# Optimization experiments

Hardware: AMD Instinct MI355X
Metric: run time of the kernel (lower is better)

The kernel has to match this reference:

```python
import jax
import jax.numpy as jnp
from jax import lax
import numpy as np

EPS = 1e-5
CLASS_COUNT = 1000

# conv specs: (out_c, in_c, k, pool_stride)
_SPECS = [(8, 1, 11, 1), (32, 8, 7, 2), (64, 32, 5, 2), (64, 64, 5, 2), (128, 64, 5, 2), (128, 128, 3, 2)]


def _maxpool3(x, stride):
    return lax.reduce_window(x, -jnp.inf, lax.max, (1, 1, 3, 3), (1, 1, stride, stride), 'VALID')


def _block(x, w, gamma, beta, pool_stride):
    # tanh soft-binarized weights (mode=1, w=1)
    wq = jnp.tanh(w)
    y = lax.conv_general_dilated(x, wq, (1, 1), 'VALID', dimension_numbers=('NCHW', 'OIHW', 'NCHW'))
    y = _maxpool3(y, pool_stride)
    # BatchNorm2d in training mode: batch statistics over (N,H,W), biased var
    mu = jnp.mean(y, axis=(0, 2, 3), keepdims=True)
    var = jnp.var(y, axis=(0, 2, 3), keepdims=True)
    y = (y - mu) * lax.rsqrt(var + EPS)
    y = y * gamma.reshape(1, -1, 1, 1) + beta.reshape(1, -1, 1, 1)
    # tanh soft-binarized activation (mode=1, w=1)
    return jnp.tanh(y)


def setup_inputs() -> dict:
    key = jax.random.key(0)
    keys = jax.random.split(key, 8)
    inp = {'x': jax.random.normal(keys[0], (128, 1, 227, 227), dtype=jnp.float32)}
    for i, (oc, ic, k, _) in enumerate(_SPECS):
        fan_in = ic * k * k
        inp[f'w{i+1}'] = jax.random.normal(keys[i + 1], (oc, ic, k, k), dtype=jnp.float32) / np.sqrt(fan_in)
        inp[f'g{i+1}'] = jnp.ones((oc,), dtype=jnp.float32)
        inp[f'b{i+1}'] = jnp.zeros((oc,), dtype=jnp.float32)
    inp['wl'] = jax.random.normal(keys[7], (CLASS_COUNT, 512), dtype=jnp.float32) / np.sqrt(512.0)
    return inp


def reference(x, w1, w2, w3, w4, w5, w6, g1, g2, g3, g4, g5, g6,
              b1, b2, b3, b4, b5, b6, wl):
    ws = (w1, w2, w3, w4, w5, w6)
    gs = (g1, g2, g3, g4, g5, g6)
    bs = (b1, b2, b3, b4, b5, b6)
    for i, (_, _, _, ps) in enumerate(_SPECS):
        x = _block(x, ws[i], gs[i], bs[i], ps)
    # flatten -> BinaryLinear (tanh-binarized weight, no bias)
    x = x.reshape(x.shape[0], -1)  # [B, 512]
    return x @ jnp.tanh(wl).T  # [B, classCount]
```

## Files before the change

kernel.cpp:

```cpp
#include <hip/hip_runtime.h>
#include <hip/hip_bf16.h>
#include <hip/hip_fp16.h>

using bf16 = __hip_bfloat16;
using f16  = _Float16;
using f16x8 = __attribute__((ext_vector_type(8))) _Float16;
using f32x4  = __attribute__((ext_vector_type(4))) float;
typedef unsigned long long u64;

__device__ __forceinline__ float b2f(bf16 v){ return __bfloat162float(v); }
__device__ __forceinline__ bf16 f2b(float v){ return __float2bfloat16(v); }
__device__ __forceinline__ float ldf(const float* p){ return *p; }
__device__ __forceinline__ float ldf(const bf16* p){ return b2f(*p); }
__device__ __forceinline__ float ldf(const __half* p){ return __half2float(*p); }
__device__ __forceinline__ void stf(float* p, float v){ *p = v; }
__device__ __forceinline__ void stf(bf16* p, float v){ *p = f2b(v); }
__device__ __forceinline__ void stf(__half* p, float v){ *p = __float2half(v); }

__device__ __forceinline__ float ftanh(float x){
    float t = __builtin_amdgcn_exp2f(x * 2.8853900817779268f);
    return 1.0f - 2.0f * __builtin_amdgcn_rcpf(t + 1.0f);
}

__device__ __forceinline__ float ld_any(const void* p, int i, int isBf16)
{
    return isBf16 ? b2f(((const bf16*)p)[i]) : ((const float*)p)[i];
}

__device__ __forceinline__ int det_bf(const void* g)
{
    return (*(const unsigned*)g == 0x3F803F80u) ? 1 : 0;
}

__device__ __forceinline__ void bn_pr(const float* __restrict__ sums,
                                      const void* __restrict__ g,
                                      const void* __restrict__ b,
                                      int bf, int C, float inv, int c,
                                      float& sc, float& sh)
{
    float mean = sums[c] * inv;
    float var  = sums[C + c] * inv - mean * mean;
    float rstd = rsqrtf(fmaxf(var, 0.f) + 1e-5f);
    sc = ld_any(g, c, bf) * rstd;
    sh = ld_any(b, c, bf) - mean * sc;
}

__global__ void xconv(const void* __restrict__ xin, float* __restrict__ xf,
                      const void* __restrict__ g1, int* __restrict__ flag, int n)
{
    int bf = det_bf(g1);
    int i = blockIdx.x * blockDim.x + threadIdx.x;
    if (i == 0) *flag = bf;
    if (i < n) xf[i] = ld_any(xin, i, bf);
}

__global__ __launch_bounds__(256)
void prep_all(const void* __restrict__ w1, const void* __restrict__ w6,
              const void* __restrict__ wlw, const void* __restrict__ w2,
              const void* __restrict__ w3, const void* __restrict__ w4,
              const void* __restrict__ w5, const void* __restrict__ g1,
              float* __restrict__ wq0, float* __restrict__ wq5,
              float* __restrict__ wlqT, __half* __restrict__ wpk,
              __half* __restrict__ wpk3, __half* __restrict__ wpk4,
              __half* __restrict__ wpk5)
{
    const int bf = det_bf(g1);
    const int b = blockIdx.x, t = threadIdx.x;
    if (b < 4) {
        int i = b * 256 + t;
        if (i < 968) wq0[i] = tanhf(ld_any(w1, i, bf));
    } else if (b < 580) {
        int i = (b - 4) * 256 + t;
        if (i < 147456) wq5[i] = tanhf(ld_any(w6, i, bf));
    } else if (b < 2580) {
        int i = (b - 580) * 256 + t;
        if (i < 512000) {
            int cls = i >> 9, k = i & 511;
            wlqT[k * 1000 + cls] = tanhf(ld_any(wlw, i, bf));
        }
    } else if (b < 2636) {
        int i = (b - 2580) * 256 + t;
        if (i < 14336) {
            int ic  = i & 7;
            int q   = (i >> 3) & 3;
            int col = (i >> 5) & 15;
            int g   = (i >> 9) & 1;
            int khg = (i >> 10) & 1;
            int kw  = i >> 11;
            int kh  = khg * 4 + q;
            int oc  = g * 16 + col;
            __half v = __float2half(0.f);
            if (kh < 7)
                v = __float2half(tanhf(ld_any(w2, (oc * 8 + ic) * 49 + kh * 7 + kw, bf)));
            wpk[i] = v;
        }
    } else if (b < 2836) {
        int i = (b - 2636) * 256 + t;
        if (i < 51200) {
            int tap = i >> 11;
            int g   = (i >> 9) & 3;
            int col = (i >> 5) & 15;
            int icp = i & 31;
            int oc  = g * 16 + col;
            wpk3[i] = __float2half(tanhf(ld_any(w3, (oc * 32 + icp) * 25 + tap, bf)));
        }
    } else if (b < 3236) {
        int i = (b - 2836) * 256 + t;
        if (i < 102400) {
            int step = i >> 11;
            int g    = (i >> 9) & 3;
            int col  = (i >> 5) & 15;
            int icp  = i & 31;
            int icg  = step / 25, tap = step - icg * 25;
            int oc   = g * 16 + col;
            int ic   = icg * 32 + icp;
            wpk4[i] = __float2half(tanhf(ld_any(w4, (oc * 64 + ic) * 25 + tap, bf)));
        }
    } else {
        int i = (b - 3236) * 256 + t;
        if (i < 204800) {
            int step = i >> 12;
            int ocg  = (i >> 11) & 1;
            int g    = (i >> 9) & 3;
            int col  = (i >> 5) & 15;
            int icp  = i & 31;
            int icg  = step / 25, tap = step - icg * 25;
            int oc   = ocg * 64 + g * 16 + col;
            int ic   = icg * 32 + icp;
            wpk5[i] = __float2half(tanhf(ld_any(w5, (oc * 64 + ic) * 25 + tap, bf)));
        }
    }
}

__global__ __launch_bounds__(256)
void b2conv(const __half* __restrict__ A1, const __half* __restrict__ wpk,
            __half* __restrict__ raw, float* __restrict__ sums2,
            const float* __restrict__ sums1, const void* __restrict__ g1,
            const void* __restrict__ b1)
{
    __shared__ __align__(16) char smem[32000];
    __shared__ float s_part[512];
    f16*   xs = (f16*)smem;
    float* pb = (float*)smem;

    const int tid = threadIdx.x;
    const int n   = blockIdx.z;
    const int ty  = blockIdx.x / 15, tx = blockIdx.x - ty * 15;
    const int cy0 = ty * 30, cx0 = tx * 14;

    const int bf1 = det_bf(g1);
    float ssc[8], ssh[8];
    #pragma unroll
    for (int j = 0; j < 8; j++)
        bn_pr(sums1, g1, b1, bf1, 8, 1.f / 5916800.f, j, ssc[j], ssh[j]);

    for (int i = tid; i < 858; i += 256) {
        int r = i / 22, c = i - r * 22;
        int gr = cy0 + r, gc = cx0 + c;
        f16x8 v = (f16x8){0, 0, 0, 0, 0, 0, 0, 0};
        if (gr < 215 && gc < 215)
            v = *(const f16x8*)((const f16*)A1 + ((size_t)(n * 215 + gr) * 215 + gc) * 8);
        f16x8 o;
        #pragma unroll
        for (int j = 0; j < 8; j++)
            o[j] = (f16)ftanh(fmaf((float)v[j], ssc[j], ssh[j]));
        *(f16x8*)(xs + i * 8) = o;
    }
    __syncthreads();

    const int lane = tid & 63, wid = tid >> 6;
    const int col = lane & 15, q = lane >> 4;
    const int arow = q * 22;

    f32x4 acc[8][2];
    #pragma unroll
    for (int f = 0; f < 8; f++)
        #pragma unroll
        for (int g = 0; g < 2; g++)
            acc[f][g] = (f32x4){0.f, 0.f, 0.f, 0.f};

    const f16* wb = (const f16*)wpk + col * 32 + q * 8;
    f16x8 wc0 = *(const f16x8*)(wb);
    f16x8 wc1 = *(const f16x8*)(wb + 512);

    #pragma unroll
    for (int s = 0; s < 14; s++) {
        f16x8 wn0 = wc0, wn1 = wc1;
        if (s < 13) {
            const f16* wn = wb + (s + 1) * 1024;
            wn0 = *(const f16x8*)(wn);
            wn1 = *(const f16x8*)(wn + 512);
        }
        int kw = s >> 1, khg = s & 1;
        int aoffs = arow + khg * 88 + kw;
        #pragma unroll
        for (int f = 0; f < 8; f++) {
            int gi = (wid * 8 + f) * 22 + col + aoffs;
            f16x8 a = *(const f16x8*)(xs + gi * 8);
            acc[f][0] = __builtin_amdgcn_mfma_f32_16x16x32_f16(a, wc0, acc[f][0], 0, 0, 0);
            acc[f][1] = __builtin_amdgcn_mfma_f32_16x16x32_f16(a, wc1, acc[f][1], 0, 0, 0);
        }
        wc0 = wn0; wc1 = wn1;
    }
    __syncthreads();

    for (int h = 0; h < 2; h++) {
        #pragma unroll
        for (int f = 0; f < 8; f++) {
            int cr = wid * 8 + f;
            if (cr < 31)
                *(f32x4*)(pb + col * 500 + cr * 16 + q * 4) = acc[f][h];
        }
        __syncthreads();
        const int ocl = tid >> 4, slot = tid & 15;
        float sm = 0.f, sq = 0.f;
        for (int j = slot; j < 105; j += 16) {
            int py = j / 7, px = j - (j / 7) * 7;
            int gph = ty * 15 + py, gpw = tx * 7 + px;
            if (gph < 104 && gpw < 104) {
                const float* cp = pb + ocl * 500 + (2 * py) * 16 + 2 * px;
                float m = cp[0];
                #pragma unroll
                for (int dy = 0; dy < 3; dy++)
                    #pragma unroll
                    for (int dx = 0; dx < 3; dx++)
                        m = fmaxf(m, cp[dy * 16 + dx]);
                int oc = h * 16 + ocl;
                size_t oidx = ((size_t)(n * 104 + gph) * 104 + gpw) * 32 + oc;
                raw[oidx] = __float2half(m);
                sm += m; sq += m * m;
            }
        }
        s_part[tid] = sm; s_part[256 + tid] = sq;
        __syncthreads();
        if (tid < 16) {
            float a = 0.f, b = 0.f;
            #pragma unroll
            for (int t = 0; t < 16; t++) {
                a += s_part[tid * 16 + t];
                b += s_part[256 + tid * 16 + t];
            }
            atomicAdd(&sums2[h * 16 + tid],      a);
            atomicAdd(&sums2[32 + h * 16 + tid], b);
        }
        __syncthreads();
    }
}

__global__ __launch_bounds__(256)
void b3conv(const __half* __restrict__ A2, const __half* __restrict__ wpk3,
            float* __restrict__ A3, float* __restrict__ sums3,
            const float* __restrict__ sums2, const void* __restrict__ g2,
            const void* __restrict__ b2)
{
    __shared__ __align__(16) char smem[32000];
    __shared__ float s_part[512];
    f16*   xs = (f16*)smem;
    float* pb = (float*)smem;

    const int tid = threadIdx.x;
    const int n   = blockIdx.z;
    const int ty  = blockIdx.x / 7, tx = blockIdx.x - ty * 7;
    const int y0  = ty * 14, x0 = tx * 14;

    if (tid < 32) {
        float sc, sh;
        bn_pr(sums2, g2, b2, det_bf(g2), 32, 1.f / 1384448.f, tid, sc, sh);
        s_part[tid] = sc; s_part[32 + tid] = sh;
    }
    __syncthreads();

    for (int i = tid; i < 1600; i += 256) {
        int pos = i >> 2, g8 = i & 3;
        int gy = y0 + pos / 20, gx = x0 + pos % 20;
        f16x8 v = *(const f16x8*)((const f16*)A2 +
                  ((size_t)(n * 104 + gy) * 104 + gx) * 32 + g8 * 8);
        int c0 = g8 * 8;
        f16x8 o;
        #pragma unroll
        for (int j = 0; j < 8; j++)
            o[j] = (f16)ftanh(fmaf((float)v[j], s_part[c0 + j], s_part[32 + c0 + j]));
        *(f16x8*)(xs + pos * 40 + g8 * 8) = o;
    }

    const int lane = tid & 63, wid = tid >> 6;
    const int col = lane & 15, q = lane >> 4;

    f32x4 acc[4][4];
    #pragma unroll
    for (int f = 0; f < 4; f++)
        #pragma unroll
        for (int g = 0; g < 4; g++)
            acc[f][g] = (f32x4){0.f, 0.f, 0.f, 0.f};

    const f16* wb = (const f16*)wpk3 + col * 32 + q * 8;
    f16x8 w[4];
    #pragma unroll
    for (int g = 0; g < 4; g++)
        w[g] = *(const f16x8*)(wb + g * 512);

    __syncthreads();

    #pragma unroll 1
    for (int tap = 0; tap < 25; tap++) {
        const f16* wnb = wb + (tap < 24 ? tap + 1 : tap) * 2048;
        f16x8 wn[4];
        #pragma unroll
        for (int g = 0; g < 4; g++)
            wn[g] = *(const f16x8*)(wnb + g * 512);

        int kh = tap / 5, kw = tap - (tap / 5) * 5;
        f16x8 a[4];
        #pragma unroll
        for (int f = 0; f < 4; f++) {
            int pos = (wid * 4 + f + kh) * 20 + col + kw;
            a[f] = *(const f16x8*)(xs + pos * 40 + q * 8);
        }
        #pragma unroll
        for (int g = 0; g < 4; g++)
            #pragma unroll
            for (int f = 0; f < 4; f++)
                acc[f][g] = __builtin_amdgcn_mfma_f32_16x16x32_f16(
                    a[f], w[g], acc[f][g], 0, 0, 0);
        #pragma unroll
        for (int g = 0; g < 4; g++)
            w[g] = wn[g];
    }

    for (int h = 0; h < 2; h++) {
        __syncthreads();
        #pragma unroll
        for (int f = 0; f < 4; f++) {
            int cr = wid * 4 + f;
            if (cr < 15) {
                #pragma unroll
                for (int gg = 0; gg < 2; gg++)
                    *(f32x4*)(pb + (gg * 16 + col) * 244 + cr * 16 + q * 4) = acc[f][h * 2 + gg];
            }
        }
        __syncthreads();
        const int ocl = tid >> 3, slot = tid & 7;
        float sm = 0.f, sq = 0.f;
        for (int j = slot; j < 49; j += 8) {
            int py = j / 7, px = j - (j / 7) * 7;
            const float* cp = pb + ocl * 244 + (2 * py) * 16 + 2 * px;
            float m = cp[0];
            #pragma unroll
            for (int dy = 0; dy < 3; dy++)
                #pragma unroll
                for (int dx = 0; dx < 3; dx++)
                    m = fmaxf(m, cp[dy * 16 + dx]);
            A3[((size_t)(n * 64 + h * 32 + ocl) * 49 + ty * 7 + py) * 49 + tx * 7 + px] = m;
            sm += m; sq += m * m;
        }
        s_part[tid] = sm; s_part[256 + tid] = sq;
        __syncthreads();
        if (tid < 32) {
            float a = 0.f, b = 0.f;
            #pragma unroll
            for (int t = 0; t < 8; t++) {
                a += s_part[tid * 8 + t];
                b += s_part[256 + tid * 8 + t];
            }
            atomicAdd(&sums3[h * 32 + tid],      a);
            atomicAdd(&sums3[64 + h * 32 + tid], b);
        }
    }
}

__global__ __launch_bounds__(256)
void bn_tanh_h_t(const float* __restrict__ x, __half* __restrict__ out,
                 const float* __restrict__ sums3, const void* __restrict__ g3,
                 const void* __restrict__ b3)
{
    __shared__ float tile[64][50];
    __shared__ float s_ss[128];
    const int tid = threadIdx.x;
    const int h = blockIdx.x % 49;
    const int n = blockIdx.x / 49;
    const int c = tid >> 2, j = tid & 3;
    if (tid < 64) {
        float sc, sh;
        bn_pr(sums3, g3, b3, det_bf(g3), 64, 1.f / 307328.f, tid, sc, sh);
        s_ss[tid] = sc; s_ss[64 + tid] = sh;
    }
    const float* xp = x + ((size_t)(n * 64 + c) * 49 + h) * 49;
    for (int w = j; w < 49; w += 4)
        tile[c][w] = xp[w];
    __syncthreads();
    __half* op = out + ((size_t)(n * 49 + h) * 49) * 64;
    for (int pos = tid; pos < 49 * 64; pos += 256) {
        int w = pos >> 6, cc = pos & 63;
        op[pos] = __float2half(ftanh(fmaf(tile[cc][w], s_ss[cc], s_ss[64 + cc])));
    }
}

__global__ __launch_bounds__(256)
void bn4_apply(const float* __restrict__ x, __half* __restrict__ out,
               const float* __restrict__ sums4, const void* __restrict__ g4,
               const void* __restrict__ b4)
{
    __shared__ float s_ss[128];
    int tid = threadIdx.x;
    if (tid < 64) {
        float sc, sh;
        bn_pr(sums4, g4, b4, det_bf(g4), 64, 1.f / 61952.f, tid, sc, sh);
        s_ss[tid] = sc; s_ss[64 + tid] = sh;
    }
    __syncthreads();
    int idx = blockIdx.x * 256 + tid;
    if (idx >= 3964928) return;
    int w  = idx % 22;
    int t1 = idx / 22;
    int h  = t1 % 22;
    int t2 = t1 / 22;
    int c  = t2 & 63;
    int n  = t2 >> 6;
    float t = ftanh(fmaf(x[idx], s_ss[c], s_ss[64 + c]));
    out[((size_t)(n * 22 + h) * 22 + w) * 64 + c] = __float2half(t);
}

__global__ __launch_bounds__(256)
void b4conv(const __half* __restrict__ A3t, const __half* __restrict__ wpk4,
            float* __restrict__ A4, float* __restrict__ sums4)
{
    __shared__ __align__(16) char smem[31232];
    __shared__ float s_part[512];
    f16*   xs = (f16*)smem;
    float* pb = (float*)smem;

    const int tid = threadIdx.x;
    const int n   = blockIdx.z;
    const int ty  = blockIdx.x >> 2, tx = blockIdx.x & 3;
    const int y0  = ty * 14, x0 = tx * 14;
    const int lane = tid & 63, wid = tid >> 6;
    const int col = lane & 15, q = lane >> 4;

    f32x4 acc[4][4];
    #pragma unroll
    for (int f = 0; f < 4; f++)
        #pragma unroll
        for (int g = 0; g < 4; g++)
            acc[f][g] = (f32x4){0.f, 0.f, 0.f, 0.f};

    const f16* wb = (const f16*)wpk4 + col * 32 + q * 8;
    f16x8 w[4];
    #pragma unroll
    for (int g = 0; g < 4; g++)
        w[g] = *(const f16x8*)(wb + g * 512);

    #pragma unroll 1
    for (int icg = 0; icg < 2; icg++) {
        __syncthreads();
        for (int i = tid; i < 1520; i += 256) {
            int pos = i >> 2, g8 = i & 3;
            int gy = y0 + pos / 20, gx = x0 + pos % 20;
            f16x8 v = (f16x8){0, 0, 0, 0, 0, 0, 0, 0};
            if (gy < 49 && gx < 49)
                v = *(const f16x8*)((const f16*)A3t +
                    ((size_t)(n * 49 + gy) * 49 + gx) * 64 + icg * 32 + g8 * 8);
            *(f16x8*)(xs + pos * 40 + g8 * 8) = v;
        }
        __syncthreads();

        #pragma unroll 1
        for (int tap = 0; tap < 25; tap++) {
            int step = icg * 25 + tap;
            const f16* wnb = wb + (size_t)(step < 49 ? step + 1 : step) * 2048;
            f16x8 wn[4];
            #pragma unroll
            for (int g = 0; g < 4; g++)
                wn[g] = *(const f16x8*)(wnb + g * 512);

            int kh = tap / 5, kw = tap - (tap / 5) * 5;
            f16x8 a[4];
            #pragma unroll
            for (int f = 0; f < 4; f++) {
                int r = wid * 4 + f + kh; if (r > 18) r = 18;
                int pos = r * 20 + col + kw;
                a[f] = *(const f16x8*)(xs + pos * 40 + q * 8);
            }
            #pragma unroll
            for (int g = 0; g < 4; g++)
                #pragma unroll
                for (int f = 0; f < 4; f++)
                    acc[f][g] = __builtin_amdgcn_mfma_f32_16x16x32_f16(
                        a[f], w[g], acc[f][g], 0, 0, 0);
            #pragma unroll
            for (int g = 0; g < 4; g++)
                w[g] = wn[g];
        }
    }

    for (int h = 0; h < 2; h++) {
        __syncthreads();
        #pragma unroll
        for (int f = 0; f < 4; f++) {
            int cr = wid * 4 + f;
            if (cr < 15) {
                #pragma unroll
                for (int gg = 0; gg < 2; gg++)
                    *(f32x4*)(pb + (gg * 16 + col) * 244 + cr * 16 + q * 4) = acc[f][h * 2 + gg];
            }
        }
        __syncthreads();
        const int ocl = tid >> 3, slot = tid & 7;
        float sm = 0.f, sq = 0.f;
        for (int j = slot; j < 49; j += 8) {
            int py = j / 7, px = j - (j / 7) * 7;
            int gph = ty * 7 + py, gpw = tx * 7 + px;
            if (gph < 22 && gpw < 22) {
                const float* cp = pb + ocl * 244 + (2 * py) * 16 + 2 * px;
                float m = cp[0];
                #pragma unroll
                for (int dy = 0; dy < 3; dy++)
                    #pragma unroll
                    for (int dx = 0; dx < 3; dx++)
                        m = fmaxf(m, cp[dy * 16 + dx]);
                A4[((size_t)(n * 64 + h * 32 + ocl) * 22 + gph) * 22 + gpw] = m;
                sm += m; sq += m * m;
            }
        }
        s_part[tid] = sm; s_part[256 + tid] = sq;
        __syncthreads();
        if (tid < 32) {
            float a = 0.f, b = 0.f;
            #pragma unroll
            for (int t = 0; t < 8; t++) {
                a += s_part[tid * 8 + t];
                b += s_part[256 + tid * 8 + t];
            }
            atomicAdd(&sums4[h * 32 + tid],      a);
            atomicAdd(&sums4[64 + h * 32 + tid], b);
        }
    }
}

__global__ __launch_bounds__(256)
void b5conv(const __half* __restrict__ A4t, const __half* __restrict__ wpk5,
            float* __restrict__ A5, float* __restrict__ sums5)
{
    __shared__ __align__(16) char smem[49664];
    __shared__ float s_part[512];
    f16*   xs = (f16*)smem;
    float* pb = (float*)smem;

    const int tid = threadIdx.x;
    const int n   = blockIdx.z;
    const int ocg = blockIdx.x;
    const int lane = tid & 63, wid = tid >> 6;
    const int col = lane & 15, q = lane >> 4;

    int abase[6];
    #pragma unroll
    for (int f = 0; f < 6; f++) {
        int m = (wid * 6 + f) * 16 + col;
        if (m > 323) m = 323;
        int r = m / 18, cc = m - r * 18;
        abase[f] = r * 22 + cc;
    }

    f32x4 acc[6][4];
    #pragma unroll
    for (int f = 0; f < 6; f++)
        #pragma unroll
        for (int g = 0; g < 4; g++)
            acc[f][g] = (f32x4){0.f, 0.f, 0.f, 0.f};

    const f16* wb = (const f16*)wpk5 + ocg * 2048 + col * 32 + q * 8;
    f16x8 w[4];
    #pragma unroll
    for (int g = 0; g < 4; g++)
        w[g] = *(const f16x8*)(wb + g * 512);

    #pragma unroll 1
    for (int icg = 0; icg < 2; icg++) {
        __syncthreads();
        for (int i = tid; i < 1936; i += 256) {
            int pos = i >> 2, g8 = i & 3;
            *(f16x8*)(xs + pos * 40 + g8 * 8) =
                *(const f16x8*)((const f16*)A4t + ((size_t)(n * 484 + pos)) * 64
                                + icg * 32 + g8 * 8);
        }
        __syncthreads();

        #pragma unroll 1
        for (int tap = 0; tap < 25; tap++) {
            int step = icg * 25 + tap;
            const f16* wnb = wb + (size_t)(step < 49 ? step + 1 : step) * 4096;
            f16x8 wn[4];
            #pragma unroll
            for (int g = 0; g < 4; g++)
                wn[g] = *(const f16x8*)(wnb + g * 512);

            int kh = tap / 5, kw = tap - (tap / 5) * 5;
            int off = kh * 22 + kw;
            f16x8 a[6];
            #pragma unroll
            for (int f = 0; f < 6; f++)
                a[f] = *(const f16x8*)(xs + (abase[f] + off) * 40 + q * 8);
            #pragma unroll
            for (int g = 0; g < 4; g++)
                #pragma unroll
                for (int f = 0; f < 6; f++)
                    acc[f][g] = __builtin_amdgcn_mfma_f32_16x16x32_f16(
                        a[f], w[g], acc[f][g], 0, 0, 0);
            #pragma unroll
            for (int g = 0; g < 4; g++)
                w[g] = wn[g];
        }
    }

    for (int h = 0; h < 2; h++) {
        __syncthreads();
        #pragma unroll
        for (int f = 0; f < 6; f++)
            #pragma unroll
            for (int gg = 0; gg < 2; gg++)
                *(f32x4*)(pb + (gg * 16 + col) * 388 + (wid * 6 + f) * 16 + q * 4)
                    = acc[f][h * 2 + gg];
        __syncthreads();
        const int ocl = tid >> 3, slot = tid & 7;
        float sm = 0.f, sq = 0.f;
        for (int j = slot; j < 64; j += 8) {
            int py = j >> 3, px = j & 7;
            const float* cp = pb + ocl * 388 + (2 * py) * 18 + 2 * px;
            float m = cp[0];
            #pragma unroll
            for (int dy = 0; dy < 3; dy++)
                #pragma unroll
                for (int dx = 0; dx < 3; dx++)
                    m = fmaxf(m, cp[dy * 18 + dx]);
            int oc = ocg * 64 + h * 32 + ocl;
            A5[((size_t)(n * 128 + oc) * 8 + py) * 8 + px] = m;
            sm += m; sq += m * m;
        }
        s_part[tid] = sm; s_part[256 + tid] = sq;
        __syncthreads();
        if (tid < 32) {
            float a = 0.f, b = 0.f;
            #pragma unroll
            for (int t = 0; t < 8; t++) {
                a += s_part[tid * 8 + t];
                b += s_part[256 + tid * 8 + t];
            }
            int oc = ocg * 64 + h * 32 + tid;
            atomicAdd(&sums5[oc],       a);
            atomicAdd(&sums5[128 + oc], b);
        }
    }
}

template<int MODE, int IC, int OC, int K, int PS, int TPH, int TPW,
         int OCB, int OCT, int CIC, int NP, bool ONHWC, typename InT, typename OutT>
__global__ __launch_bounds__(256)
void ctile(const InT* __restrict__ in, const float* __restrict__ wq,
           OutT* __restrict__ out, float* __restrict__ sums,
           const float* __restrict__ ss,
           int Hin, int Win, int PH, int PW, int tilesX)
{
    constexpr int TPO  = OCB / OCT;
    constexpr int CH   = PS * (TPH - 1) + 3;
    constexpr int CW   = PS * (TPW - 1) + 3;
    constexpr int SPR  = (CW + NP - 1) / NP;
    constexpr int CWP  = SPR * NP;
    constexpr int NSTR = CH * SPR;
    static_assert(NSTR * TPO <= 256, "thread mapping overflow");
    constexpr int IH   = CH + K - 1;
    constexpr int IW   = CW + K - 1;
    constexpr int IWE_ = (CWP + K - 1 > IW) ? (CWP + K - 1) : IW;
    constexpr int IWE  = IWE_ | 1;
    constexpr int IN_SZ  = CIC * IH * IWE;
    constexpr int INP    = (IN_SZ + 3) & ~3;
    constexpr int W_SZ   = CIC * K * K * OCB;
    constexpr int CONV_SZ = OCB * CH * CWP;
    constexpr int LDS_SZ = (INP + W_SZ > CONV_SZ) ? (INP + W_SZ) : CONV_SZ;

    __shared__ __align__(16) float lds[LDS_SZ];
    __shared__ float s_part[512];

    const int tid = threadIdx.x;
    const int n   = blockIdx.z;
    const int oc0 = blockIdx.y * OCB;
    const int tY  = blockIdx.x / tilesX;
    const int tX  = blockIdx.x - tY * tilesX;
    const int ph0 = tY * TPH, pw0 = tX * TPW;
    const int ih0 = ph0 * PS, iw0 = pw0 * PS;

    const int  og  = tid % TPO;
    const int  s   = tid / TPO;
    const bool act = (s < NSTR);
    const int  r   = s / SPR;
    const int  c0  = (s - r * SPR) * NP;

    float acc[NP][OCT];
    #pragma unroll
    for (int p = 0; p < NP; p++)
        #pragma unroll
        for (int o = 0; o < OCT; o++) acc[p][o] = 0.f;

    for (int icb = 0; icb < IC; icb += CIC) {
        for (int idx = tid; idx < IN_SZ; idx += 256) {
            int ic  = idx / (IH * IWE);
            int rem = idx - ic * (IH * IWE);
            int rr  = rem / IWE, cc = rem - rr * IWE;
            int gr  = ih0 + rr, gc = iw0 + cc;
            float v = 0.f;
            if (gr < Hin && gc < Win)
                v = ldf(&in[((size_t)(n * IC + icb + ic) * Hin + gr) * Win + gc]);
            lds[idx] = v;
        }
        for (int idx = tid; idx < W_SZ; idx += 256) {
            int ocl = idx % OCB;
            int kk  = (idx / OCB) % (K * K);
            int c_  = idx / (OCB * K * K);
            lds[INP + idx] = wq[((size_t)(oc0 + ocl) * IC + icb + c_) * (K * K) + kk];
        }
        __syncthreads();

        if (act) {
            #pragma unroll 1
            for (int ic_ = 0; ic_ < CIC; ic_++) {
                const float* xb = lds + ic_ * (IH * IWE);
                const float* wb = lds + INP + ic_ * (K * K * OCB) + og * OCT;
                #pragma unroll 1
                for (int kh = 0; kh < K; kh++) {
                    const float* xr = xb + (r + kh) * IWE + c0;
                    float xwin[NP + K - 1];
                    #pragma unroll
                    for (int j = 0; j < NP + K - 1; j++) xwin[j] = xr[j];
                    #pragma unroll
                    for (int kw = 0; kw < K; kw++) {
                        const float* wp2 = wb + (kh * K + kw) * OCB;
                        float wv[OCT];
                        #pragma unroll
                        for (int o = 0; o < OCT; o += 4) {
                            float4 t = *(const float4*)(wp2 + o);
                            wv[o] = t.x; wv[o+1] = t.y; wv[o+2] = t.z; wv[o+3] = t.w;
                        }
                        #pragma unroll
                        for (int p = 0; p < NP; p++)
                            #pragma unroll
                            for (int o = 0; o < OCT; o++)
                                acc[p][o] = fmaf(wv[o], xwin[p + kw], acc[p][o]);
                    }
                }
            }
        }
        __syncthreads();
    }

    if (act) {
        #pragma unroll
        for (int p = 0; p < NP; p++)
            #pragma unroll
            for (int o = 0; o < OCT; o++)
                lds[(og * OCT + o) * (CH * CWP) + r * CWP + c0 + p] = acc[p][o];
    }
    __syncthreads();

    {
        constexpr int TPC = 256 / OCB;
        const int ocl = tid / TPC, slot = tid - ocl * TPC;
        float sm = 0.f, sq = 0.f;
        for (int j = slot; j < TPH * TPW; j += TPC) {
            int py = j / TPW, px = j - (j / TPW) * TPW;
            int gph = ph0 + py, gpw = pw0 + px;
            if (gph < PH && gpw < PW) {
                const float* cp = lds + ocl * (CH * CWP) + (py * PS) * CWP + px * PS;
                float m = cp[0];
                #pragma unroll
                for (int dy = 0; dy < 3; dy++)
                    #pragma unroll
                    for (int dx = 0; dx < 3; dx++)
                        m = fmaxf(m, cp[dy * CWP + dx]);
                size_t oidx = ONHWC
                    ? ((size_t)(n * PH + gph) * PW + gpw) * OC + oc0 + ocl
                    : ((size_t)(n * OC + oc0 + ocl) * PH + gph) * PW + gpw;
                if (MODE == 2) {
                    int c = oc0 + ocl;
                    stf(&out[oidx], ftanh(fmaf(m, ss[c], ss[OC + c])));
                } else {
                    if (MODE == 0) stf(&out[oidx], m);
                    sm += m; sq += m * m;
                }
            }
        }
        if (MODE != 2) {
            s_part[tid] = sm; s_part[256 + tid] = sq;
            __syncthreads();
            if (tid < OCB) {
                float a = 0.f, b = 0.f;
// ... 87 lines not shown
    __shared__ float ls[256], ls2[256];
    ls[threadIdx.x] = s; ls2[threadIdx.x] = s2;
    __syncthreads();
    for (int w = 128; w > 0; w >>= 1) {
        if (threadIdx.x < w) {
            ls[threadIdx.x]  += ls[threadIdx.x + w];
            ls2[threadIdx.x] += ls2[threadIdx.x + w];
        }
        __syncthreads();
    }
    if (threadIdx.x == 0) {
        atomicAdd(&sums[c],     ls[0]);
        atomicAdd(&sums[C + c], ls2[0]);
    }
}

__global__ __launch_bounds__(256)
void bn_tanh_p(float* __restrict__ x, const float* __restrict__ sums,
               const void* __restrict__ g, const void* __restrict__ b,
               int C, int PHW, float invCnt)
{
    int plane = blockIdx.y;
    int c = plane & (C - 1);
    float sc, sh;
    bn_pr(sums, g, b, det_bf(g), C, invCnt, c, sc, sh);
    float* xp = x + (long)plane * PHW;
    for (int i = blockIdx.x * 256 + threadIdx.x; i < PHW; i += 256 * gridDim.x)
        xp[i] = ftanh(fmaf(xp[i], sc, sh));
}

__global__ __launch_bounds__(256)
void linear_k(const float* __restrict__ act, const float* __restrict__ wlqT,
              void* __restrict__ out, const int* __restrict__ flag)
{
    __shared__ float s_a[512];
    int bf = *flag;
    int n = blockIdx.y;
    for (int i = threadIdx.x; i < 512; i += 256) s_a[i] = act[n * 512 + i];
    __syncthreads();
    int cls = blockIdx.x * 256 + threadIdx.x;
    if (cls < 1000) {
        float acc = 0.f;
        #pragma unroll 8
        for (int k = 0; k < 512; k++)
            acc = fmaf(s_a[k], wlqT[k * 1000 + cls], acc);
        if (bf) ((bf16*)out)[n * 1000 + cls] = f2b(acc);
        else    ((float*)out)[n * 1000 + cls] = acc;
    }
}

extern "C" void kernel_launch(void* const* d_in, const int* in_sizes, int n_in,
                              void* d_out, int out_size, void* d_ws, size_t ws_size,
                              hipStream_t stream)
{
    (void)in_sizes; (void)n_in; (void)out_size; (void)ws_size;
    const void* x = d_in[0];
    const void* W[6]; const void* G[6]; const void* B[6];
    for (int i = 0; i < 6; i++) {
        W[i] = d_in[1 + 3 * i];
        G[i] = d_in[2 + 3 * i];
        B[i] = d_in[3 + 3 * i];
    }
    const void* wl = d_in[19];

    char* p = (char*)d_ws;
    auto carve = [&](size_t bytes) -> void* {
        void* r = (void*)p;
        p += (bytes + 255) & ~((size_t)255);
        return r;
    };
    int*   flag = (int*)carve(256);
    const int wsz[6] = {968, 12544, 51200, 102400, 204800, 147456};
    float* wq[6];
    for (int i = 0; i < 6; i++) wq[i] = (float*)carve((size_t)wsz[i] * 4);
    float* wlqT = (float*)carve((size_t)512000 * 4);
    float* sums_all = (float*)carve(1536 * 4);
    float* S1 = sums_all;        float* S2 = sums_all + 256;
    float* S3 = sums_all + 512;  float* S4 = sums_all + 768;
    float* S5 = sums_all + 1024; float* S6 = sums_all + 1280;
    __half* wpk  = (__half*)carve((size_t)14336 * 2);
    __half* wpk3 = (__half*)carve((size_t)51200 * 2);
    __half* wpk4 = (__half*)carve((size_t)102400 * 2);
    __half* wpk5 = (__half*)carve((size_t)204800 * 2);
    float* xf   = (float*)carve((size_t)6595712 * 4);
    __half* A1  = (__half*)carve((size_t)47334400 * 2);
    __half* A2  = (__half*)carve((size_t)44302336 * 2);
    float*  A3  = (float*)A1;
    __half* A3t = (__half*)A2;
    float*  A4  = (float*)A1;
    float*  A5  = (float*)A2;
    __half* A4t = (__half*)((char*)A2 + (size_t)16 * 1024 * 1024);
    float*  A6  = (float*)A1;

    auto cdiv = [](int a, int b) { return (a + b - 1) / b; };

    hipMemsetAsync(sums_all, 0, 1536 * 4, stream);
    xconv<<<cdiv(6595712, 256), 256, 0, stream>>>(x, xf, G[0], flag, 6595712);
    prep_all<<<4036, 256, 0, stream>>>(W[0], W[5], wl, W[1], W[2], W[3], W[4], G[0],
                                       wq[0], wq[5], wlqT, wpk, wpk3, wpk4, wpk5);

    ctile<0, 1, 8, 11, 1, 34, 40, 8, 8, 1, 7, true, float, __half>
        <<<dim3(42, 1, 128), 256, 0, stream>>>(xf, wq[0], A1, S1, S1, 227, 227, 215, 215, 6);

    b2conv<<<dim3(105, 1, 128), 256, 0, stream>>>(A1, wpk, A2, S2, S1, G[0], B[0]);

    b3conv<<<dim3(49, 1, 128), 256, 0, stream>>>(A2, wpk3, A3, S3, S2, G[1], B[1]);
    bn_tanh_h_t<<<128 * 49, 256, 0, stream>>>(A3, A3t, S3, G[2], B[2]);

    b4conv<<<dim3(16, 1, 128), 256, 0, stream>>>(A3t, wpk4, A4, S4);
    bn4_apply<<<cdiv(3964928, 256), 256, 0, stream>>>(A4, A4t, S4, G[3], B[3]);

    b5conv<<<dim3(2, 1, 128), 256, 0, stream>>>(A4t, wpk5, A5, S5);
    bn_tanh_p<<<dim3(1, 16384), 256, 0, stream>>>(A5, S5, G[4], B[4], 128, 64, 1.f / 8192.f);

    {
        int total = 65536;
        convpool<3, 0, float, float><<<cdiv(total, 256), 256, 0, stream>>>(
            A5, wq[5], A6, S6, 128, 128, 2, 8, 8, 2, 2, total);
        stats_k<float><<<128, 256, 0, stream>>>(A6, S6, 128, 128, 4, 1);
        bn_tanh_p<<<dim3(1, 16384), 256, 0, stream>>>(A6, S6, G[5], B[5], 128, 4, 1.f / 512.f);
    }
    linear_k<<<dim3(4, 128), 256, 0, stream>>>(A6, wlqT, d_out, flag);
}
```

Measured before the change: 1.373 ms.

## Drop input conversion pass and stage conv epilogues in fp16 shared memory

Removes the standalone xconv kernel: the first conv tile now reads the raw input directly, with an in-kernel dtype check, and the bf16 flag is written by prep_all instead. In the b2–b5 conv kernels the pre-pool accumulator staging buffer is stored as fp16 rather than fp32, so all channel halves fit at once and the two-pass epilogue with extra barriers collapses into a single pass. Intermediate activations A3 and A4 are stored as half instead of float, halving their memory traffic, and the downstream BN kernels read half. Rounding conv outputs to fp16 before max-pooling and before the batch statistics are taken reduces precision.

```diff
diff --git a/kernel.cpp b/kernel.cpp
--- a/kernel.cpp
+++ b/kernel.cpp
@@ -4,6 +4,7 @@
 
 using bf16 = __hip_bfloat16;
 using f16  = _Float16;
+using f16x4 = __attribute__((ext_vector_type(4))) _Float16;
 using f16x8 = __attribute__((ext_vector_type(8))) _Float16;
 using f32x4  = __attribute__((ext_vector_type(4))) float;
 typedef unsigned long long u64;
@@ -45,15 +46,6 @@
     sh = ld_any(b, c, bf) - mean * sc;
 }
 
-__global__ void xconv(const void* __restrict__ xin, float* __restrict__ xf,
-                      const void* __restrict__ g1, int* __restrict__ flag, int n)
-{
-    int bf = det_bf(g1);
-    int i = blockIdx.x * blockDim.x + threadIdx.x;
-    if (i == 0) *flag = bf;
-    if (i < n) xf[i] = ld_any(xin, i, bf);
-}
-
 __global__ __launch_bounds__(256)
 void prep_all(const void* __restrict__ w1, const void* __restrict__ w6,
               const void* __restrict__ wlw, const void* __restrict__ w2,
@@ -62,10 +54,11 @@
               float* __restrict__ wq0, float* __restrict__ wq5,
               float* __restrict__ wlqT, __half* __restrict__ wpk,
               __half* __restrict__ wpk3, __half* __restrict__ wpk4,
-              __half* __restrict__ wpk5)
+              __half* __restrict__ wpk5, int* __restrict__ flag)
 {
     const int bf = det_bf(g1);
     const int b = blockIdx.x, t = threadIdx.x;
+    if (b == 0 && t == 0) *flag = bf;
     if (b < 4) {
         int i = b * 256 + t;
         if (i < 968) wq0[i] = tanhf(ld_any(w1, i, bf));
@@ -140,8 +133,8 @@
 {
     __shared__ __align__(16) char smem[32000];
     __shared__ float s_part[512];
-    f16*   xs = (f16*)smem;
-    float* pb = (float*)smem;
+    f16*  xs   = (f16*)smem;
+    f16*  pb16 = (f16*)smem;
 
     const int tid = threadIdx.x;
     const int n   = blockIdx.z;
@@ -204,59 +197,65 @@
     }
     __syncthreads();
 
-    for (int h = 0; h < 2; h++) {
-        #pragma unroll
-        for (int f = 0; f < 8; f++) {
-            int cr = wid * 8 + f;
-            if (cr < 31)
-                *(f32x4*)(pb + col * 500 + cr * 16 + q * 4) = acc[f][h];
-        }
-        __syncthreads();
-        const int ocl = tid >> 4, slot = tid & 15;
+    #pragma unroll
+    for (int f = 0; f < 8; f++) {
+        int cr = wid * 8 + f;
+        if (cr < 31) {
+            #pragma unroll
+            for (int g = 0; g < 2; g++) {
+                f16x4 hv;
+                #pragma unroll
+                for (int j = 0; j < 4; j++) hv[j] = (f16)acc[f][g][j];
+                *(f16x4*)(pb16 + (g * 16 + col) * 500 + cr * 16 + q * 4) = hv;
+            }
+        }
+    }
+    __syncthreads();
+
+    {
+        const int ocl = tid >> 3, slot = tid & 7;
         float sm = 0.f, sq = 0.f;
-        for (int j = slot; j < 105; j += 16) {
+        for (int j = slot; j < 105; j += 8) {
             int py = j / 7, px = j - (j / 7) * 7;
             int gph = ty * 15 + py, gpw = tx * 7 + px;
             if (gph < 104 && gpw < 104) {
-                const float* cp = pb + ocl * 500 + (2 * py) * 16 + 2 * px;
-                float m = cp[0];
+                const f16* cp = pb16 + ocl * 500 + (2 * py) * 16 + 2 * px;
+                float m = (float)cp[0];
                 #pragma unroll
                 for (int dy = 0; dy < 3; dy++)
                     #pragma unroll
                     for (int dx = 0; dx < 3; dx++)
-                        m = fmaxf(m, cp[dy * 16 + dx]);
-                int oc = h * 16 + ocl;
-                size_t oidx = ((size_t)(n * 104 + gph) * 104 + gpw) * 32 + oc;
+                        m = fmaxf(m, (float)cp[dy * 16 + dx]);
+                size_t oidx = ((size_t)(n * 104 + gph) * 104 + gpw) * 32 + ocl;
                 raw[oidx] = __float2half(m);
                 sm += m; sq += m * m;
             }
         }
         s_part[tid] = sm; s_part[256 + tid] = sq;
         __syncthreads();
-        if (tid < 16) {
+        if (tid < 32) {
             float a = 0.f, b = 0.f;
             #pragma unroll
-            for (int t = 0; t < 16; t++) {
-                a += s_part[tid * 16 + t];
-                b += s_part[256 + tid * 16 + t];
-            }
-            atomicAdd(&sums2[h * 16 + tid],      a);
-            atomicAdd(&sums2[32 + h * 16 + tid], b);
-        }
-        __syncthreads();
+            for (int t = 0; t < 8; t++) {
+                a += s_part[tid * 8 + t];
+                b += s_part[256 + tid * 8 + t];
+            }
+            atomicAdd(&sums2[tid],      a);
+            atomicAdd(&sums2[32 + tid], b);
+        }
     }
 }
 
 __global__ __launch_bounds__(256)
 void b3conv(const __half* __restrict__ A2, const __half* __restrict__ wpk3,
-            float* __restrict__ A3, float* __restrict__ sums3,
+            __half* __restrict__ A3, float* __restrict__ sums3,
             const float* __restrict__ sums2, const void* __restrict__ g2,
             const void* __restrict__ b2)
 {
     __shared__ __align__(16) char smem[32000];
     __shared__ float s_part[512];
-    f16*   xs = (f16*)smem;
-    float* pb = (float*)smem;
+    f16*  xs   = (f16*)smem;
+    f16*  pb16 = (f16*)smem;
 
     const int tid = threadIdx.x;
     const int n   = blockIdx.z;
@@ -327,49 +326,55 @@
             w[g] = wn[g];
     }
 
-    for (int h = 0; h < 2; h++) {
-        __syncthreads();
-        #pragma unroll
-        for (int f = 0; f < 4; f++) {
-            int cr = wid * 4 + f;
-            if (cr < 15) {
-                #pragma unroll
-                for (int gg = 0; gg < 2; gg++)
-                    *(f32x4*)(pb + (gg * 16 + col) * 244 + cr * 16 + q * 4) = acc[f][h * 2 + gg];
-            }
-        }
-        __syncthreads();
-        const int ocl = tid >> 3, slot = tid & 7;
+    __syncthreads();
+
+    #pragma unroll
+    for (int f = 0; f < 4; f++) {
+        int cr = wid * 4 + f;
+        if (cr < 15) {
+            #pragma unroll
+            for (int g = 0; g < 4; g++) {
+                f16x4 hv;
+                #pragma unroll
+                for (int j = 0; j < 4; j++) hv[j] = (f16)acc[f][g][j];
+                *(f16x4*)(pb16 + (g * 16 + col) * 244 + cr * 16 + q * 4) = hv;
+            }
+        }
+    }
+    __syncthreads();
+
+    {
+        const int ocl = tid >> 2, slot = tid & 3;
         float sm = 0.f, sq = 0.f;
-        for (int j = slot; j < 49; j += 8) {
+        for (int j = slot; j < 49; j += 4) {
             int py = j / 7, px = j - (j / 7) * 7;
-            const float* cp = pb + ocl * 244 + (2 * py) * 16 + 2 * px;
-            float m = cp[0];
+            const f16* cp = pb16 + ocl * 244 + (2 * py) * 16 + 2 * px;
+            float m = (float)cp[0];
             #pragma unroll
             for (int dy = 0; dy < 3; dy++)
                 #pragma unroll
                 for (int dx = 0; dx < 3; dx++)
-                    m = fmaxf(m, cp[dy * 16 + dx]);
-            A3[((size_t)(n * 64 + h * 32 + ocl) * 49 + ty * 7 + py) * 49 + tx * 7 + px] = m;
+                    m = fmaxf(m, (float)cp[dy * 16 + dx]);
+            A3[((size_t)(n * 64 + ocl) * 49 + ty * 7 + py) * 49 + tx * 7 + px] = __float2half(m);
             sm += m; sq += m * m;
         }
         s_part[tid] = sm; s_part[256 + tid] = sq;
         __syncthreads();
-        if (tid < 32) {
+        if (tid < 64) {
             float a = 0.f, b = 0.f;
             #pragma unroll
-            for (int t = 0; t < 8; t++) {
-                a += s_part[tid * 8 + t];
-                b += s_part[256 + tid * 8 + t];
-            }
-            atomicAdd(&sums3[h * 32 + tid],      a);
-            atomicAdd(&sums3[64 + h * 32 + tid], b);
-        }
-    }
-}
-
-__global__ __launch_bounds__(256)
-void bn_tanh_h_t(const float* __restrict__ x, __half* __restrict__ out,
+            for (int t = 0; t < 4; t++) {
+                a += s_part[tid * 4 + t];
+                b += s_part[256 + tid * 4 + t];
+            }
+            atomicAdd(&sums3[tid],      a);
+            atomicAdd(&sums3[64 + tid], b);
+        }
+    }
+}
+
+__global__ __launch_bounds__(256)
+void bn_tanh_h_t(const __half* __restrict__ x, __half* __restrict__ out,
                  const float* __restrict__ sums3, const void* __restrict__ g3,
                  const void* __restrict__ b3)
 {
@@ -384,9 +389,9 @@
         bn_pr(sums3, g3, b3, det_bf(g3), 64, 1.f / 307328.f, tid, sc, sh);
         s_ss[tid] = sc; s_ss[64 + tid] = sh;
     }
-    const float* xp = x + ((size_t)(n * 64 + c) * 49 + h) * 49;
+    const __half* xp = x + ((size_t)(n * 64 + c) * 49 + h) * 49;
     for (int w = j; w < 49; w += 4)
-        tile[c][w] = xp[w];
+        tile[c][w] = __half2float(xp[w]);
     __syncthreads();
     __half* op = out + ((size_t)(n * 49 + h) * 49) * 64;
     for (int pos = tid; pos < 49 * 64; pos += 256) {
@@ -396,7 +401,7 @@
 }
 
 __global__ __launch_bounds__(256)
-void bn4_apply(const float* __restrict__ x, __half* __restrict__ out,
+void bn4_apply(const __half* __restrict__ x, __half* __restrict__ out,
                const float* __restrict__ sums4, const void* __restrict__ g4,
                const void* __restrict__ b4)
 {
@@ -416,18 +421,18 @@
     int t2 = t1 / 22;
     int c  = t2 & 63;
     int n  = t2 >> 6;
-    float t = ftanh(fmaf(x[idx], s_ss[c], s_ss[64 + c]));
+    float t = ftanh(fmaf(__half2float(x[idx]), s_ss[c], s_ss[64 + c]));
     out[((size_t)(n * 22 + h) * 22 + w) * 64 + c] = __float2half(t);
 }
 
 __global__ __launch_bounds__(256)
 void b4conv(const __half* __restrict__ A3t, const __half* __restrict__ wpk4,
-            float* __restrict__ A4, float* __restrict__ sums4)
+            __half* __restrict__ A4, float* __restrict__ sums4)
 {
     __shared__ __align__(16) char smem[31232];
     __shared__ float s_part[512];
-    f16*   xs = (f16*)smem;
-    float* pb = (float*)smem;
+    f16*  xs   = (f16*)smem;
+    f16*  pb16 = (f16*)smem;
 
     const int tid = threadIdx.x;
     const int n   = blockIdx.z;
@@ -492,46 +497,52 @@
         }
     }
 
-    for (int h = 0; h < 2; h++) {
-        __syncthreads();
-        #pragma unroll
-        for (int f = 0; f < 4; f++) {
-            int cr = wid * 4 + f;
-            if (cr < 15) {
-                #pragma unroll
-                for (int gg = 0; gg < 2; gg++)
-                    *(f32x4*)(pb + (gg * 16 + col) * 244 + cr * 16 + q * 4) = acc[f][h * 2 + gg];
-            }
-        }
-        __syncthreads();
-        const int ocl = tid >> 3, slot = tid & 7;
+    __syncthreads();
+
+    #pragma unroll
+    for (int f = 0; f < 4; f++) {
+        int cr = wid * 4 + f;
+        if (cr < 15) {
+            #pragma unroll
+            for (int g = 0; g < 4; g++) {
+                f16x4 hv;
+                #pragma unroll
+                for (int j = 0; j < 4; j++) hv[j] = (f16)acc[f][g][j];
+                *(f16x4*)(pb16 + (g * 16 + col) * 244 + cr * 16 + q * 4) = hv;
+            }
+        }
+    }
+    __syncthreads();
+
+    {
+        const int ocl = tid >> 2, slot = tid & 3;
         float sm = 0.f, sq = 0.f;
-        for (int j = slot; j < 49; j += 8) {
+        for (int j = slot; j < 49; j += 4) {
             int py = j / 7, px = j - (j / 7) * 7;
             int gph = ty * 7 + py, gpw = tx * 7 + px;
             if (gph < 22 && gpw < 22) {
-                const float* cp = pb + ocl * 244 + (2 * py) * 16 + 2 * px;
-                float m = cp[0];
+                const f16* cp = pb16 + ocl * 244 + (2 * py) * 16 + 2 * px;
+                float m = (float)cp[0];
                 #pragma unroll
                 for (int dy = 0; dy < 3; dy++)
                     #pragma unroll
                     for (int dx = 0; dx < 3; dx++)
-                        m = fmaxf(m, cp[dy * 16 + dx]);
-                A4[((size_t)(n * 64 + h * 32 + ocl) * 22 + gph) * 22 + gpw] = m;
+                        m = fmaxf(m, (float)cp[dy * 16 + dx]);
+                A4[((size_t)(n * 64 + ocl) * 22 + gph) * 22 + gpw] = __float2half(m);
                 sm += m; sq += m * m;
             }
         }
         s_part[tid] = sm; s_part[256 + tid] = sq;
         __syncthreads();
-        if (tid < 32) {
+        if (tid < 64) {
             float a = 0.f, b = 0.f;
             #pragma unroll
-            for (int t = 0; t < 8; t++) {
-                a += s_part[tid * 8 + t];
-                b += s_part[256 + tid * 8 + t];
-            }
-            atomicAdd(&sums4[h * 32 + tid],      a);
-            atomicAdd(&sums4[64 + h * 32 + tid], b);
+            for (int t = 0; t < 4; t++) {
+                a += s_part[tid * 4 + t];
+                b += s_part[256 + tid * 4 + t];
+            }
+            atomicAdd(&sums4[tid],      a);
+            atomicAdd(&sums4[64 + tid], b);
         }
     }
 }
@@ -542,8 +553,8 @@
 {
     __shared__ __align__(16) char smem[49664];
     __shared__ float s_part[512];
-    f16*   xs = (f16*)smem;
-    float* pb = (float*)smem;
+    f16*  xs   = (f16*)smem;
+    f16*  pb16 = (f16*)smem;
 
     const int tid = threadIdx.x;
     const int n   = blockIdx.z;
@@ -611,52 +622,57 @@
         }
     }
 
-    for (int h = 0; h < 2; h++) {
-        __syncthreads();
-        #pragma unroll
-        for (int f = 0; f < 6; f++)
-            #pragma unroll
-            for (int gg = 0; gg < 2; gg++)
-                *(f32x4*)(pb + (gg * 16 + col) * 388 + (wid * 6 + f) * 16 + q * 4)
-                    = acc[f][h * 2 + gg];
-        __syncthreads();
-        const int ocl = tid >> 3, slot = tid & 7;
+    __syncthreads();
+
+    #pragma unroll
+    for (int f = 0; f < 6; f++)
+        #pragma unroll
+        for (int g = 0; g < 4; g++) {
+            f16x4 hv;
+            #pragma unroll
+            for (int j = 0; j < 4; j++) hv[j] = (f16)acc[f][g][j];
+            *(f16x4*)(pb16 + (g * 16 + col) * 388 + (wid * 6 + f) * 16 + q * 4) = hv;
+        }
+    __syncthreads();
+
+    {
+        const int ocl = tid >> 2, slot = tid & 3;
         float sm = 0.f, sq = 0.f;
-        for (int j = slot; j < 64; j += 8) {
+        for (int j = slot; j < 64; j += 4) {
             int py = j >> 3, px = j & 7;
-            const float* cp = pb + ocl * 388 + (2 * py) * 18 + 2 * px;
-            float m = cp[0];
+            const f16* cp = pb16 + ocl * 388 + (2 * py) * 18 + 2 * px;
+            float m = (float)cp[0];
             #pragma unroll
             for (int dy = 0; dy < 3; dy++)
                 #pragma unroll
                 for (int dx = 0; dx < 3; dx++)
-                    m = fmaxf(m, cp[dy * 18 + dx]);
-            int oc = ocg * 64 + h * 32 + ocl;
+                    m = fmaxf(m, (float)cp[dy * 18 + dx]);
+            int oc = ocg * 64 + ocl;
             A5[((size_t)(n * 128 + oc) * 8 + py) * 8 + px] = m;
             sm += m; sq += m * m;
         }
         s_part[tid] = sm; s_part[256 + tid] = sq;
         __syncthreads();
-        if (tid < 32) {
+        if (tid < 64) {
             float a = 0.f, b = 0.f;
             #pragma unroll
-            for (int t = 0; t < 8; t++) {
-                a += s_part[tid * 8 + t];
-                b += s_part[256 + tid * 8 + t];
-            }
-            int oc = ocg * 64 + h * 32 + tid;
+            for (int t = 0; t < 4; t++) {
+                a += s_part[tid * 4 + t];
+                b += s_part[256 + tid * 4 + t];
+            }
+            int oc = ocg * 64 + tid;
             atomicAdd(&sums5[oc],       a);
             atomicAdd(&sums5[128 + oc], b);
         }
     }
 }
 
-template<int MODE, int IC, int OC, int K, int PS, int TPH, int TPW,
+template<int MODE, int RAWIN, int IC, int OC, int K, int PS, int TPH, int TPW,
          int OCB, int OCT, int CIC, int NP, bool ONHWC, typename InT, typename OutT>
 __global__ __launch_bounds__(256)
-void ctile(const InT* __restrict__ in, const float* __restrict__ wq,
+void ctile(const void* __restrict__ in, const float* __restrict__ wq,
            OutT* __restrict__ out, float* __restrict__ sums,
-           const float* __restrict__ ss,
+           const float* __restrict__ ss, const void* __restrict__ g1in,
            int Hin, int Win, int PH, int PW, int tilesX)
 {
     constexpr int TPO  = OCB / OCT;
@@ -687,6 +703,8 @@
     const int ph0 = tY * TPH, pw0 = tX * TPW;
     const int ih0 = ph0 * PS, iw0 = pw0 * PS;
 
+    const int bfin = RAWIN ? det_bf(g1in) : 0;
+
     const int  og  = tid % TPO;
     const int  s   = tid / TPO;
     const bool act = (s < NSTR);
@@ -706,8 +724,10 @@
             int rr  = rem / IWE, cc = rem - rr * IWE;
             int gr  = ih0 + rr, gc = iw0 + cc;
             float v = 0.f;
-            if (gr < Hin && gc < Win)
-                v = ldf(&in[((size_t)(n * IC + icb + ic) * Hin + gr) * Win + gc]);
+            if (gr < Hin && gc < Win) {
+                size_t gidx = ((size_t)(n * IC + icb + ic) * Hin + gr) * Win + gc;
+                v = RAWIN ? ld_any(in, (int)gidx, bfin) : ldf(&((const InT*)in)[gidx]);
+            }
             lds[idx] = v;
         }
         for (int idx = tid; idx < W_SZ; idx += 256) {
@@ -961,12 +981,11 @@
     __half* wpk3 = (__half*)carve((size_t)51200 * 2);
     __half* wpk4 = (__half*)carve((size_t)102400 * 2);
     __half* wpk5 = (__half*)carve((size_t)204800 * 2);
-    float* xf   = (float*)carve((size_t)6595712 * 4);
     __half* A1  = (__half*)carve((size_t)47334400 * 2);
     __half* A2  = (__half*)carve((size_t)44302336 * 2);
-    float*  A3  = (float*)A1;
+    __half* A3  = (__half*)A1;
     __half* A3t = (__half*)A2;
-    float*  A4  = (float*)A1;
+    __half* A4  = (__half*)A1;
     float*  A5  = (float*)A2;
     __half* A4t = (__half*)((char*)A2 + (size_t)16 * 1024 * 1024);
     float*  A6  = (float*)A1;
@@ -974,12 +993,11 @@
     auto cdiv = [](int a, int b) { return (a + b - 1) / b; };
 
     hipMemsetAsync(sums_all, 0, 1536 * 4, stream);
-    xconv<<<cdiv(6595712, 256), 256, 0, stream>>>(x, xf, G[0], flag, 6595712);
     prep_all<<<4036, 256, 0, stream>>>(W[0], W[5], wl, W[1], W[2], W[3], W[4], G[0],
-                                       wq[0], wq[5], wlqT, wpk, wpk3, wpk4, wpk5);
-
-    ctile<0, 1, 8, 11, 1, 34, 40, 8, 8, 1, 7, true, float, __half>
-        <<<dim3(42, 1, 128), 256, 0, stream>>>(xf, wq[0], A1, S1, S1, 227, 227, 215, 215, 6);
+                                       wq[0], wq[5], wlqT, wpk, wpk3, wpk4, wpk5, flag);
+
+    ctile<0, 1, 1, 8, 11, 1, 34, 40, 8, 8, 1, 7, true, float, __half>
+        <<<dim3(42, 1, 128), 256, 0, stream>>>(x, wq[0], A1, S1, S1, G[0], 227, 227, 215, 215, 6);
 
     b2conv<<<dim3(105, 1, 128), 256, 0, stream>>>(A1, wpk, A2, S2, S1, G[0], B[0]);
 
```

New measurement: 1.410 ms. 2.7% more time.

## Drop input conversion kernel and store conv3/conv4 pooled outputs as fp16

Applied to the files above, without the earlier changes.

Removes the separate xconv pass that copied the raw input into a float buffer. The first conv tile kernel now reads the raw input directly, detecting bf16 versus fp32 itself, and the flag write moves into prep_all. The pre-BN pooled outputs of b3conv and b4conv are stored as fp16 instead of fp32, roughly halving those intermediate writes and the reads in the BN apply kernels. BN statistics are still accumulated in fp32 before rounding, but the normalized values are now computed from fp16-rounded activations, which adds a small precision risk.

```diff
diff --git a/kernel.cpp b/kernel.cpp
--- a/kernel.cpp
+++ b/kernel.cpp
@@ -45,15 +45,6 @@
     sh = ld_any(b, c, bf) - mean * sc;
 }
 
-__global__ void xconv(const void* __restrict__ xin, float* __restrict__ xf,
-                      const void* __restrict__ g1, int* __restrict__ flag, int n)
-{
-    int bf = det_bf(g1);
-    int i = blockIdx.x * blockDim.x + threadIdx.x;
-    if (i == 0) *flag = bf;
-    if (i < n) xf[i] = ld_any(xin, i, bf);
-}
-
 __global__ __launch_bounds__(256)
 void prep_all(const void* __restrict__ w1, const void* __restrict__ w6,
               const void* __restrict__ wlw, const void* __restrict__ w2,
@@ -62,10 +53,11 @@
               float* __restrict__ wq0, float* __restrict__ wq5,
               float* __restrict__ wlqT, __half* __restrict__ wpk,
               __half* __restrict__ wpk3, __half* __restrict__ wpk4,
-              __half* __restrict__ wpk5)
+              __half* __restrict__ wpk5, int* __restrict__ flag)
 {
     const int bf = det_bf(g1);
     const int b = blockIdx.x, t = threadIdx.x;
+    if (b == 0 && t == 0) *flag = bf;
     if (b < 4) {
         int i = b * 256 + t;
         if (i < 968) wq0[i] = tanhf(ld_any(w1, i, bf));
@@ -249,7 +241,7 @@
 
 __global__ __launch_bounds__(256)
 void b3conv(const __half* __restrict__ A2, const __half* __restrict__ wpk3,
-            float* __restrict__ A3, float* __restrict__ sums3,
+            __half* __restrict__ A3, float* __restrict__ sums3,
             const float* __restrict__ sums2, const void* __restrict__ g2,
             const void* __restrict__ b2)
 {
@@ -350,7 +342,8 @@
                 #pragma unroll
                 for (int dx = 0; dx < 3; dx++)
                     m = fmaxf(m, cp[dy * 16 + dx]);
-            A3[((size_t)(n * 64 + h * 32 + ocl) * 49 + ty * 7 + py) * 49 + tx * 7 + px] = m;
+            A3[((size_t)(n * 64 + h * 32 + ocl) * 49 + ty * 7 + py) * 49 + tx * 7 + px]
+                = __float2half(m);
             sm += m; sq += m * m;
         }
         s_part[tid] = sm; s_part[256 + tid] = sq;
@@ -369,7 +362,7 @@
 }
 
 __global__ __launch_bounds__(256)
-void bn_tanh_h_t(const float* __restrict__ x, __half* __restrict__ out,
+void bn_tanh_h_t(const __half* __restrict__ x, __half* __restrict__ out,
                  const float* __restrict__ sums3, const void* __restrict__ g3,
                  const void* __restrict__ b3)
 {
@@ -384,9 +377,9 @@
         bn_pr(sums3, g3, b3, det_bf(g3), 64, 1.f / 307328.f, tid, sc, sh);
         s_ss[tid] = sc; s_ss[64 + tid] = sh;
     }
-    const float* xp = x + ((size_t)(n * 64 + c) * 49 + h) * 49;
+    const __half* xp = x + ((size_t)(n * 64 + c) * 49 + h) * 49;
     for (int w = j; w < 49; w += 4)
-        tile[c][w] = xp[w];
+        tile[c][w] = __half2float(xp[w]);
     __syncthreads();
     __half* op = out + ((size_t)(n * 49 + h) * 49) * 64;
     for (int pos = tid; pos < 49 * 64; pos += 256) {
@@ -396,7 +389,7 @@
 }
 
 __global__ __launch_bounds__(256)
-void bn4_apply(const float* __restrict__ x, __half* __restrict__ out,
+void bn4_apply(const __half* __restrict__ x, __half* __restrict__ out,
                const float* __restrict__ sums4, const void* __restrict__ g4,
                const void* __restrict__ b4)
 {
@@ -416,13 +409,13 @@
     int t2 = t1 / 22;
     int c  = t2 & 63;
     int n  = t2 >> 6;
-    float t = ftanh(fmaf(x[idx], s_ss[c], s_ss[64 + c]));
+    float t = ftanh(fmaf(__half2float(x[idx]), s_ss[c], s_ss[64 + c]));
     out[((size_t)(n * 22 + h) * 22 + w) * 64 + c] = __float2half(t);
 }
 
 __global__ __launch_bounds__(256)
 void b4conv(const __half* __restrict__ A3t, const __half* __restrict__ wpk4,
-            float* __restrict__ A4, float* __restrict__ sums4)
+            __half* __restrict__ A4, float* __restrict__ sums4)
 {
     __shared__ __align__(16) char smem[31232];
     __shared__ float s_part[512];
@@ -517,7 +510,8 @@
                     #pragma unroll
                     for (int dx = 0; dx < 3; dx++)
                         m = fmaxf(m, cp[dy * 16 + dx]);
-                A4[((size_t)(n * 64 + h * 32 + ocl) * 22 + gph) * 22 + gpw] = m;
+                A4[((size_t)(n * 64 + h * 32 + ocl) * 22 + gph) * 22 + gpw]
+                    = __float2half(m);
                 sm += m; sq += m * m;
             }
         }
@@ -651,12 +645,12 @@
     }
 }
 
-template<int MODE, int IC, int OC, int K, int PS, int TPH, int TPW,
+template<int MODE, int RAWIN, int IC, int OC, int K, int PS, int TPH, int TPW,
          int OCB, int OCT, int CIC, int NP, bool ONHWC, typename InT, typename OutT>
 __global__ __launch_bounds__(256)
-void ctile(const InT* __restrict__ in, const float* __restrict__ wq,
+void ctile(const void* __restrict__ in, const float* __restrict__ wq,
            OutT* __restrict__ out, float* __restrict__ sums,
-           const float* __restrict__ ss,
+           const float* __restrict__ ss, const void* __restrict__ g1in,
            int Hin, int Win, int PH, int PW, int tilesX)
 {
     constexpr int TPO  = OCB / OCT;
@@ -687,6 +681,8 @@
     const int ph0 = tY * TPH, pw0 = tX * TPW;
     const int ih0 = ph0 * PS, iw0 = pw0 * PS;
 
+    const int bfin = RAWIN ? det_bf(g1in) : 0;
+
     const int  og  = tid % TPO;
     const int  s   = tid / TPO;
     const bool act = (s < NSTR);
@@ -706,8 +702,10 @@
             int rr  = rem / IWE, cc = rem - rr * IWE;
             int gr  = ih0 + rr, gc = iw0 + cc;
             float v = 0.f;
-            if (gr < Hin && gc < Win)
-                v = ldf(&in[((size_t)(n * IC + icb + ic) * Hin + gr) * Win + gc]);
+            if (gr < Hin && gc < Win) {
+                size_t gidx = ((size_t)(n * IC + icb + ic) * Hin + gr) * Win + gc;
+                v = RAWIN ? ld_any(in, (int)gidx, bfin) : ldf(&((const InT*)in)[gidx]);
+            }
             lds[idx] = v;
         }
         for (int idx = tid; idx < W_SZ; idx += 256) {
@@ -961,12 +959,11 @@
     __half* wpk3 = (__half*)carve((size_t)51200 * 2);
     __half* wpk4 = (__half*)carve((size_t)102400 * 2);
     __half* wpk5 = (__half*)carve((size_t)204800 * 2);
-    float* xf   = (float*)carve((size_t)6595712 * 4);
     __half* A1  = (__half*)carve((size_t)47334400 * 2);
     __half* A2  = (__half*)carve((size_t)44302336 * 2);
-    float*  A3  = (float*)A1;
+    __half* A3  = (__half*)A1;
     __half* A3t = (__half*)A2;
-    float*  A4  = (float*)A1;
+    __half* A4  = (__half*)A1;
     float*  A5  = (float*)A2;
     __half* A4t = (__half*)((char*)A2 + (size_t)16 * 1024 * 1024);
     float*  A6  = (float*)A1;
@@ -974,12 +971,11 @@
     auto cdiv = [](int a, int b) { return (a + b - 1) / b; };
 
     hipMemsetAsync(sums_all, 0, 1536 * 4, stream);
-    xconv<<<cdiv(6595712, 256), 256, 0, stream>>>(x, xf, G[0], flag, 6595712);
     prep_all<<<4036, 256, 0, stream>>>(W[0], W[5], wl, W[1], W[2], W[3], W[4], G[0],
-                                       wq[0], wq[5], wlqT, wpk, wpk3, wpk4, wpk5);
-
-    ctile<0, 1, 8, 11, 1, 34, 40, 8, 8, 1, 7, true, float, __half>
-        <<<dim3(42, 1, 128), 256, 0, stream>>>(xf, wq[0], A1, S1, S1, 227, 227, 215, 215, 6);
+                                       wq[0], wq[5], wlqT, wpk, wpk3, wpk4, wpk5, flag);
+
+    ctile<0, 1, 1, 8, 11, 1, 34, 40, 8, 8, 1, 7, true, float, __half>
+        <<<dim3(42, 1, 128), 256, 0, stream>>>(x, wq[0], A1, S1, S1, G[0], 227, 227, 215, 215, 6);
 
     b2conv<<<dim3(105, 1, 128), 256, 0, stream>>>(A1, wpk, A2, S2, S1, G[0], B[0]);
 
```

New measurement: 1.342 ms. -2.3%, faster.
